# Kernel tuning notes

Measured on AMD Instinct MI355X. Metric: run time of the kernel, lower is better.

The kernel has to match this reference:

```python
import jax, jax.numpy as jnp
import numpy as np

GAMMA = 1.0

def _rbf_mean(a, b, gamma):
    # mean of exp(-gamma * ||a_i - b_j||^2) over the full [Na, Nb] kernel matrix
    aa = jnp.sum(a * a, axis=1, keepdims=True)          # [Na, 1]
    bb = jnp.sum(b * b, axis=1, keepdims=True)          # [Nb, 1]
    dist = aa + bb.T - 2.0 * (a @ b.T)                  # [Na, Nb]
    return jnp.mean(jnp.exp(-gamma * dist))

def setup_inputs() -> dict:
    key = jax.random.key(0)
    kx, ky = jax.random.split(key)
    N, D = 8192, 128
    x = jax.random.normal(kx, (N, D), dtype=jnp.float32)
    y = jax.random.normal(ky, (N, D), dtype=jnp.float32)
    return {"x": x, "y": y}

def reference(x, y):
    mmd = (_rbf_mean(x, x, GAMMA)
           + _rbf_mean(y, y, GAMMA)
           - 2.0 * _rbf_mean(x, y, GAMMA))
    return mmd
```

## Files before the change

kernel.cpp:

```cpp
#include <hip/hip_runtime.h>


#define N_PTS 8192
#define DCOLS 128
#define TILE 128
#define TJ 64
#define NSELF 2080
#define NJOBS 8256
#define NBLOCKS 768
#define LOG2E 1.4426950408889634f
#define THRESH -40.0f
#define QS 24.0f
#define INV_S2 (1.0f / (QS * QS))

typedef __attribute__((ext_vector_type(4))) int int4v;
typedef unsigned int u32;
typedef unsigned short u16;
typedef unsigned char u8;

#if __has_builtin(__builtin_amdgcn_exp2f)
#define EXP2(x) __builtin_amdgcn_exp2f(x)
#else
#define EXP2(x) exp2f(x)
#endif

__device__ __forceinline__ void gl_lds16(const u8* g, u8* l) {
  __builtin_amdgcn_global_load_lds(
      (const __attribute__((address_space(1))) u32*)g,
      (__attribute__((address_space(3))) u32*)l, 16, 0, 0);
}

__global__ void prep_kernel(const float* __restrict__ x, const float* __restrict__ y,
                            u16* __restrict__ xb, u16* __restrict__ yb,
                            float* __restrict__ da, float* __restrict__ db,
                            u32* __restrict__ Sz) {
  if (blockIdx.x == 0 && threadIdx.x < 4) Sz[threadIdx.x] = 0;
  int wid = threadIdx.x >> 6;
  int lane = threadIdx.x & 63;
  int row = blockIdx.x * 4 + wid;
  const float* src;
  u16* dst;
  float* dn;
  int r;
  if (row < N_PTS) { src = x; dst = xb; dn = da; r = row; }
  else             { src = y; dst = yb; dn = db; r = row - N_PTS; }
  float2 v = ((const float2*)(src + (size_t)r * 128))[lane];
  int q0 = (int)rintf(fminf(fmaxf(v.x * QS, -127.f), 127.f));
  int q1 = (int)rintf(fminf(fmaxf(v.y * QS, -127.f), 127.f));
  dst[(size_t)r * 64 + lane] = (u16)((q0 & 0xff) | ((q1 & 0xff) << 8));
  int p = q0 * q0 + q1 * q1;
#pragma unroll
  for (int off = 32; off; off >>= 1) p += __shfl_down(p, off, 64);
  if (lane == 0) dn[r] = -LOG2E * INV_S2 * (float)p;
}

struct Job { int pair, rr, cc; };

__device__ __forceinline__ Job decode_job(int t) {
  Job jb;
  if (t < 2 * NSELF) {
    jb.pair = (t < NSELF) ? 0 : 1;
    int tt = t - jb.pair * NSELF;
    int r = 0;
    while (tt >= TJ - r) { tt -= TJ - r; r++; }
    jb.rr = r; jb.cc = r + tt;
  } else {
    int q = t - 2 * NSELF;
    jb.pair = 2; jb.rr = q >> 6; jb.cc = q & 63;
  }
  return jb;
}

__device__ __forceinline__ Job next_job(Job c) {
  Job n = c;
  if (c.pair == 2) {
    if (c.cc == 63) { n.rr++; n.cc = 0; } else n.cc++;
  } else {
    if (c.cc == 63) {
      if (c.rr == 63) { n.pair++; n.rr = 0; n.cc = 0; }
      else { n.rr++; n.cc = n.rr; }
    } else n.cc++;
  }
  return n;
}

__device__ __forceinline__ void pair_ptrs(int pair, const u8* xb, const u8* yb,
                                          const float* da, const float* db,
                                          const u8*& A, const u8*& B,
                                          const float*& dA, const float*& dB) {
  A = (pair == 1) ? yb : xb;
  B = (pair == 0) ? xb : yb;
  dA = (pair == 1) ? db : da;
  dB = (pair == 0) ? da : db;
}

__device__ __forceinline__ void stage_tile(const u8* gsrc, u8* ldst,
                                           int wid, int lane) {
  int r8 = lane >> 3, c7 = lane & 7;
  const u8* gl = gsrc + r8 * DCOLS + ((c7 ^ r8) << 4);
#pragma unroll
  for (int i = 0; i < 4; i++) {
    int blk = wid * 4 + i;
    gl_lds16(gl + blk * 1024, ldst + blk * 1024);
  }
}

__device__ __forceinline__ void load_afrags(const u8* gA, const float* gdA, int rr,
                                            int mbase, int quad, int l15,
                                            int4v afr[2][4], float dam[16]) {
  const u8* base = gA + (size_t)rr * (TILE * DCOLS);
#pragma unroll
  for (int ks = 0; ks < 2; ks++)
#pragma unroll
    for (int mi = 0; mi < 4; mi++)
      afr[ks][mi] = *(const int4v*)(base + (mbase + mi * 16 + l15) * DCOLS +
                                    ks * 64 + quad * 16);
  const float* dr = gdA + rr * TILE + mbase;
#pragma unroll
  for (int mi = 0; mi < 4; mi++)
#pragma unroll
    for (int v = 0; v < 4; v++) dam[mi * 4 + v] = dr[mi * 16 + quad * 4 + v];
}

__global__ __launch_bounds__(256, 3) void mmd_kernel(
    const u8* __restrict__ xb, const u8* __restrict__ yb,
    const float* __restrict__ da, const float* __restrict__ db,
    float* __restrict__ S, u32* __restrict__ cnt, float* __restrict__ out) {
  __shared__ __align__(16) u8 Bt[2][TILE * DCOLS];

  int tid = threadIdx.x;
  int wid = tid >> 6, lane = tid & 63;
  int quad = lane >> 4, l15 = lane & 15;
  int mbase = (wid >> 1) * 64, nbase = (wid & 1) * 64;

  int start = (int)(((u32)blockIdx.x * NJOBS) / NBLOCKS);
  int end = (int)(((u32)(blockIdx.x + 1) * NJOBS) / NBLOCKS);

  Job cur = decode_job(start);
  const u8 *cA, *cB;
  const float *cdA, *cdB;
  pair_ptrs(cur.pair, xb, yb, da, db, cA, cB, cdA, cdB);

  int4v afr[2][4];
  float dam[16];
  load_afrags(cA, cdA, cur.rr, mbase, quad, l15, afr, dam);
  stage_tile(cB + (size_t)cur.cc * (TILE * DCOLS), &Bt[0][0], wid, lane);
  __syncthreads();

  const float c1 = 2.0f * LOG2E * INV_S2;
  float tsum = 0.f;
  int p = 0;

  for (int j = start; j < end; j++) {
    bool hasNext = (j + 1 < end);
    Job nxt;
    const u8 *nA = cA, *nB = cB;
    const float *ndA = cdA, *ndB = cdB;

    float dbn[4];
    {
      const float* dr = cdB + cur.cc * TILE + nbase;
#pragma unroll
      for (int ni = 0; ni < 4; ni++) dbn[ni] = dr[ni * 16 + l15];
    }

    if (hasNext) {
      nxt = next_job(cur);
      pair_ptrs(nxt.pair, xb, yb, da, db, nA, nB, ndA, ndB);
      stage_tile(nB + (size_t)nxt.cc * (TILE * DCOLS), &Bt[p ^ 1][0], wid, lane);
    }

    int4v acc[4][4];
    int4v zero = {0, 0, 0, 0};
#pragma unroll
    for (int mi = 0; mi < 4; mi++)
#pragma unroll
      for (int ni = 0; ni < 4; ni++) acc[mi][ni] = zero;

#pragma unroll
    for (int ks = 0; ks < 2; ks++) {
      int4v bf[4];
      int slot = ((ks * 4 + quad) ^ (l15 & 7)) << 4;
#pragma unroll
      for (int ni = 0; ni < 4; ni++) {
        int row = nbase + ni * 16 + l15;
        bf[ni] = *(const int4v*)(&Bt[p][row * DCOLS + slot]);
      }
#pragma unroll
      for (int mi = 0; mi < 4; mi++)
#pragma unroll
        for (int ni = 0; ni < 4; ni++)
          acc[mi][ni] = __builtin_amdgcn_mfma_i32_16x16x64_i8(
              afr[ks][mi], bf[ni], acc[mi][ni], 0, 0, 0);
    }

    float w = (cur.pair < 2 && cur.rr != cur.cc) ? 2.0f : 1.0f;
#pragma unroll
    for (int mi = 0; mi < 4; mi++) {
#pragma unroll
      for (int ni = 0; ni < 4; ni++) {
        float tv0 = fmaf(c1, (float)acc[mi][ni][0], dam[mi * 4 + 0]);
        float tv1 = fmaf(c1, (float)acc[mi][ni][1], dam[mi * 4 + 1]);
        float tv2 = fmaf(c1, (float)acc[mi][ni][2], dam[mi * 4 + 2]);
        float tv3 = fmaf(c1, (float)acc[mi][ni][3], dam[mi * 4 + 3]);
        float mx = fmaxf(fmaxf(tv0, tv1), fmaxf(tv2, tv3)) + dbn[ni];
        if (__any(mx > THRESH)) {
          float e = EXP2(tv0 + dbn[ni]) + EXP2(tv1 + dbn[ni]) +
                    EXP2(tv2 + dbn[ni]) + EXP2(tv3 + dbn[ni]);
          tsum = fmaf(w, e, tsum);
        }
      }
    }

    bool flush = !hasNext || (nxt.pair != cur.pair);
    if (flush) {
      float r = tsum;
#pragma unroll
      for (int off = 32; off; off >>= 1) r += __shfl_down(r, off, 64);
      if (lane == 0) atomicAdd(&S[cur.pair], r);
      tsum = 0.f;
    }

    if (hasNext && (nxt.pair != cur.pair || nxt.rr != cur.rr))
      load_afrags(nA, ndA, nxt.rr, mbase, quad, l15, afr, dam);

    __syncthreads();
    p ^= 1;
    if (hasNext) { cur = nxt; cA = nA; cB = nB; cdA = ndA; cdB = ndB; }
  }

  __syncthreads();
  if (tid == 0) {
    __threadfence();
    u32 old = atomicAdd(cnt, 1u);
    if (old == (u32)(NBLOCKS - 1)) {
      float s0 = atomicAdd(&S[0], 0.0f);
      float s1 = atomicAdd(&S[1], 0.0f);
      float s2 = atomicAdd(&S[2], 0.0f);
      out[0] = (s0 + s1 - 2.0f * s2) * (1.0f / ((float)N_PTS * (float)N_PTS));
    }
  }
}

extern "C" void kernel_launch(void* const* d_in, const int* in_sizes, int n_in,
                              void* d_out, int out_size, void* d_ws, size_t ws_size,
                              hipStream_t stream) {
  const float* x = (const float*)d_in[0];
  const float* y = (const float*)d_in[1];
  char* ws = (char*)d_ws;
  float* S = (float*)ws;
  u32* cnt = (u32*)ws + 3;
  u8* xb = (u8*)(ws + 256);
  u8* yb = (u8*)(ws + 256 + (1 << 20));
  float* da = (float*)(ws + 256 + (2 << 20));
  float* db = (float*)(ws + 256 + (2 << 20) + 32768);

  prep_kernel<<<4096, 256, 0, stream>>>(x, y, (u16*)xb, (u16*)yb, da, db, (u32*)ws);
  mmd_kernel<<<NBLOCKS, 256, 0, stream>>>(xb, yb, da, db, S, cnt, (float*)d_out);
}
```

Baseline: 129.1 us.

## Drop LDS double-buffered B staging; load B fragments directly from global

Removes the LDS double buffer and global_load_lds staging of B tiles, so each wave now loads its B fragments straight from global/L2 into registers, and the per-iteration __syncthreads goes away. The early-exit test now uses an integer max of the accumulator plus a per-row max of the A norms, with the exact A norms reloaded only when the bound passes. This cuts register pressure (16 dam floats become 4) and removes barriers. In exchange, loads are no longer prefetched a tile ahead, so the MFMAs may stall on global latency, and B data is re-read by both wave rows instead of being shared through LDS.

```diff
diff --git a/kernel.cpp b/kernel.cpp
--- a/kernel.cpp
+++ b/kernel.cpp
@@ -23,12 +23,6 @@
 #else
 #define EXP2(x) exp2f(x)
 #endif
-
-__device__ __forceinline__ void gl_lds16(const u8* g, u8* l) {
-  __builtin_amdgcn_global_load_lds(
-      (const __attribute__((address_space(1))) u32*)g,
-      (__attribute__((address_space(3))) u32*)l, 16, 0, 0);
-}
 
 __global__ void prep_kernel(const float* __restrict__ x, const float* __restrict__ y,
                             u16* __restrict__ xb, u16* __restrict__ yb,
@@ -94,20 +88,9 @@
   dB = (pair == 0) ? da : db;
 }
 
-__device__ __forceinline__ void stage_tile(const u8* gsrc, u8* ldst,
-                                           int wid, int lane) {
-  int r8 = lane >> 3, c7 = lane & 7;
-  const u8* gl = gsrc + r8 * DCOLS + ((c7 ^ r8) << 4);
-#pragma unroll
-  for (int i = 0; i < 4; i++) {
-    int blk = wid * 4 + i;
-    gl_lds16(gl + blk * 1024, ldst + blk * 1024);
-  }
-}
-
-__device__ __forceinline__ void load_afrags(const u8* gA, const float* gdA, int rr,
+__device__ __forceinline__ void load_astrip(const u8* gA, const float* gdA, int rr,
                                             int mbase, int quad, int l15,
-                                            int4v afr[2][4], float dam[16]) {
+                                            int4v afr[2][4], float dmx[4]) {
   const u8* base = gA + (size_t)rr * (TILE * DCOLS);
 #pragma unroll
   for (int ks = 0; ks < 2; ks++)
@@ -117,17 +100,19 @@
                                     ks * 64 + quad * 16);
   const float* dr = gdA + rr * TILE + mbase;
 #pragma unroll
-  for (int mi = 0; mi < 4; mi++)
-#pragma unroll
-    for (int v = 0; v < 4; v++) dam[mi * 4 + v] = dr[mi * 16 + quad * 4 + v];
+  for (int mi = 0; mi < 4; mi++) {
+    float d0 = dr[mi * 16 + quad * 4 + 0];
+    float d1 = dr[mi * 16 + quad * 4 + 1];
+    float d2 = dr[mi * 16 + quad * 4 + 2];
+    float d3 = dr[mi * 16 + quad * 4 + 3];
+    dmx[mi] = fmaxf(fmaxf(d0, d1), fmaxf(d2, d3));
+  }
 }
 
 __global__ __launch_bounds__(256, 3) void mmd_kernel(
     const u8* __restrict__ xb, const u8* __restrict__ yb,
     const float* __restrict__ da, const float* __restrict__ db,
     float* __restrict__ S, u32* __restrict__ cnt, float* __restrict__ out) {
-  __shared__ __align__(16) u8 Bt[2][TILE * DCOLS];
-
   int tid = threadIdx.x;
   int wid = tid >> 6, lane = tid & 63;
   int quad = lane >> 4, l15 = lane & 15;
@@ -142,20 +127,23 @@
   pair_ptrs(cur.pair, xb, yb, da, db, cA, cB, cdA, cdB);
 
   int4v afr[2][4];
-  float dam[16];
-  load_afrags(cA, cdA, cur.rr, mbase, quad, l15, afr, dam);
-  stage_tile(cB + (size_t)cur.cc * (TILE * DCOLS), &Bt[0][0], wid, lane);
-  __syncthreads();
+  float dmx[4];
+  load_astrip(cA, cdA, cur.rr, mbase, quad, l15, afr, dmx);
 
   const float c1 = 2.0f * LOG2E * INV_S2;
   float tsum = 0.f;
-  int p = 0;
 
   for (int j = start; j < end; j++) {
     bool hasNext = (j + 1 < end);
-    Job nxt;
-    const u8 *nA = cA, *nB = cB;
-    const float *ndA = cdA, *ndB = cdB;
+
+    const u8* bt = cB + (size_t)cur.cc * (TILE * DCOLS);
+    int4v bf[2][4];
+#pragma unroll
+    for (int ks = 0; ks < 2; ks++)
+#pragma unroll
+      for (int ni = 0; ni < 4; ni++)
+        bf[ks][ni] = *(const int4v*)(bt + (nbase + ni * 16 + l15) * DCOLS +
+                                     ks * 64 + quad * 16);
 
     float dbn[4];
     {
@@ -164,12 +152,6 @@
       for (int ni = 0; ni < 4; ni++) dbn[ni] = dr[ni * 16 + l15];
     }
 
-    if (hasNext) {
-      nxt = next_job(cur);
-      pair_ptrs(nxt.pair, xb, yb, da, db, nA, nB, ndA, ndB);
-      stage_tile(nB + (size_t)nxt.cc * (TILE * DCOLS), &Bt[p ^ 1][0], wid, lane);
-    }
-
     int4v acc[4][4];
     int4v zero = {0, 0, 0, 0};
 #pragma unroll
@@ -178,33 +160,29 @@
       for (int ni = 0; ni < 4; ni++) acc[mi][ni] = zero;
 
 #pragma unroll
-    for (int ks = 0; ks < 2; ks++) {
-      int4v bf[4];
-      int slot = ((ks * 4 + quad) ^ (l15 & 7)) << 4;
-#pragma unroll
-      for (int ni = 0; ni < 4; ni++) {
-        int row = nbase + ni * 16 + l15;
-        bf[ni] = *(const int4v*)(&Bt[p][row * DCOLS + slot]);
-      }
+    for (int ks = 0; ks < 2; ks++)
 #pragma unroll
       for (int mi = 0; mi < 4; mi++)
 #pragma unroll
         for (int ni = 0; ni < 4; ni++)
           acc[mi][ni] = __builtin_amdgcn_mfma_i32_16x16x64_i8(
-              afr[ks][mi], bf[ni], acc[mi][ni], 0, 0, 0);
-    }
+              afr[ks][mi], bf[ks][ni], acc[mi][ni], 0, 0, 0);
 
     float w = (cur.pair < 2 && cur.rr != cur.cc) ? 2.0f : 1.0f;
+    const float* dAex = cdA + cur.rr * TILE + mbase + quad * 4;
 #pragma unroll
     for (int mi = 0; mi < 4; mi++) {
 #pragma unroll
       for (int ni = 0; ni < 4; ni++) {
-        float tv0 = fmaf(c1, (float)acc[mi][ni][0], dam[mi * 4 + 0]);
-        float tv1 = fmaf(c1, (float)acc[mi][ni][1], dam[mi * 4 + 1]);
-        float tv2 = fmaf(c1, (float)acc[mi][ni][2], dam[mi * 4 + 2]);
-        float tv3 = fmaf(c1, (float)acc[mi][ni][3], dam[mi * 4 + 3]);
-        float mx = fmaxf(fmaxf(tv0, tv1), fmaxf(tv2, tv3)) + dbn[ni];
-        if (__any(mx > THRESH)) {
+        int4v a = acc[mi][ni];
+        int im = max(max(a[0], a[1]), max(a[2], a[3]));
+        float bound = fmaf(c1, (float)im, dmx[mi] + dbn[ni]);
+        if (__any(bound > THRESH)) {
+          const float* dv = dAex + mi * 16;
+          float tv0 = fmaf(c1, (float)a[0], dv[0]);
+          float tv1 = fmaf(c1, (float)a[1], dv[1]);
+          float tv2 = fmaf(c1, (float)a[2], dv[2]);
+          float tv3 = fmaf(c1, (float)a[3], dv[3]);
           float e = EXP2(tv0 + dbn[ni]) + EXP2(tv1 + dbn[ni]) +
                     EXP2(tv2 + dbn[ni]) + EXP2(tv3 + dbn[ni]);
           tsum = fmaf(w, e, tsum);
@@ -212,6 +190,8 @@
       }
     }
 
+    Job nxt;
+    if (hasNext) nxt = next_job(cur);
     bool flush = !hasNext || (nxt.pair != cur.pair);
     if (flush) {
       float r = tsum;
@@ -221,12 +201,13 @@
       tsum = 0.f;
     }
 
-    if (hasNext && (nxt.pair != cur.pair || nxt.rr != cur.rr))
-      load_afrags(nA, ndA, nxt.rr, mbase, quad, l15, afr, dam);
-
-    __syncthreads();
-    p ^= 1;
-    if (hasNext) { cur = nxt; cA = nA; cB = nB; cdA = ndA; cdB = ndB; }
+    if (hasNext) {
+      if (nxt.pair != cur.pair || nxt.rr != cur.rr) {
+        pair_ptrs(nxt.pair, xb, yb, da, db, cA, cB, cdA, cdB);
+        load_astrip(cA, cdA, nxt.rr, mbase, quad, l15, afr, dmx);
+      }
+      cur = nxt;
+    }
   }
 
   __syncthreads();
```

New measurement: 144.2 us. +11.6%, slower.
